# Optimization experiments

Measured on AMD Instinct MI355X. Metric: run time of the kernel, lower is better.

Reference implementation:

```python
import jax, jax.numpy as jnp
import numpy as np

E = 8      # num_expert
D = 1024   # d_model
H = 2048   # expert hidden (htoh4 size)
K = 2      # top_k
N = 2048   # tokens (batch*seq)


def setup_inputs() -> dict:
    key = jax.random.key(0)
    ks = jax.random.split(key, 4)
    sc = lambda k, shape, s: jax.random.normal(k, shape, jnp.float32) * s
    return {
        "inp": jax.random.normal(ks[0], (N, D), jnp.float32),
        "Wg": sc(ks[1], (D, E), D ** -0.5),          # NaiveGate linear
        "bg": jnp.zeros((E,), jnp.float32),
        "W1": sc(ks[2], (E, D, H), D ** -0.5),        # per-expert htoh4
        "b1": jnp.zeros((E, H), jnp.float32),
        "W2": sc(ks[3], (E, H, D), H ** -0.5),        # per-expert h4toh
        "b2": jnp.zeros((E, D), jnp.float32),
    }


def reference(inp, Wg, bg, W1, b1, W2, b2):
    # NaiveGate: linear -> top_k logits -> softmax over the k selected logits
    logits = inp @ Wg + bg                              # [N, E]
    top_val, top_idx = jax.lax.top_k(logits, K)         # [N, K]
    gate_score = jax.nn.softmax(top_val, axis=-1)       # [N, K]

    # Expert grouped compute. Reference computes every expert on every token
    # (exact math, no capacity dropping); combine selects the routed ones.
    h = jax.nn.gelu(jnp.einsum('nd,edh->neh', inp, W1) + b1)   # [N, E, H]
    y = jnp.einsum('neh,ehd->ned', h, W2) + b2                 # [N, E, D]

    # Combine: equivalent to bmm(gate_score[N,1,K], x[N,K,D]) after gather.
    comb = jnp.sum(jax.nn.one_hot(top_idx, E, dtype=inp.dtype)
                   * gate_score[..., None], axis=1)            # [N, E]
    return jnp.einsum('ne,ned->nd', comb, y)                   # [N, D]
```

## Files before the change

kernel.cpp:

```cpp
#include <hip/hip_runtime.h>
#include <math.h>

#define N_TOK 2048
#define DM    1024
#define HD    2048
#define NE    8
#define RMAX  5120
#define TMAX  40
#define KSPL  2

#define GATE_BLKS 512
#define XCVT_BLKS 1024
#define WCV2_BLKS 2048
#define PREP_BLKS (GATE_BLKS + XCVT_BLKS + WCV2_BLKS)

typedef short short8 __attribute__((ext_vector_type(8)));
typedef unsigned short u16x8 __attribute__((ext_vector_type(8)));
typedef float f32x4  __attribute__((ext_vector_type(4)));

__device__ inline unsigned short f2b(float f) {
  unsigned int u = __float_as_uint(f);
  return (unsigned short)((u + 0x7FFFu + ((u >> 16) & 1u)) >> 16);
}
__device__ inline float b2f(unsigned short s) {
  return __uint_as_float(((unsigned int)s) << 16);
}
__device__ inline void gload_lds16(const void* g, void* l) {
  __builtin_amdgcn_global_load_lds(
      (const __attribute__((address_space(1))) unsigned int*)g,
      (__attribute__((address_space(3))) unsigned int*)l, 16, 0, 0);
}

__global__ __launch_bounds__(256) void prep_kernel(
    const float* __restrict__ inp, const float* __restrict__ Wg,
    const float* __restrict__ bg,  const float* __restrict__ W2,
    int* __restrict__ top_idx, float* __restrict__ gate_w,
    unsigned short* __restrict__ Xb, unsigned short* __restrict__ W2C) {
  int bid = blockIdx.x;
  if (bid < GATE_BLKS) {
    int wave = threadIdx.x >> 6;
    int lane = threadIdx.x & 63;
    int n = bid * 4 + wave;
    float acc[NE];
#pragma unroll
    for (int e = 0; e < NE; ++e) acc[e] = 0.f;
    const float4* wg4 = reinterpret_cast<const float4*>(Wg);
#pragma unroll
    for (int i = 0; i < DM / 64; ++i) {
      int d = i * 64 + lane;
      float x = inp[n * DM + d];
      float4 w0 = wg4[d * 2 + 0];
      float4 w1 = wg4[d * 2 + 1];
      acc[0] += x * w0.x; acc[1] += x * w0.y; acc[2] += x * w0.z; acc[3] += x * w0.w;
      acc[4] += x * w1.x; acc[5] += x * w1.y; acc[6] += x * w1.z; acc[7] += x * w1.w;
    }
#pragma unroll
    for (int off = 32; off > 0; off >>= 1) {
#pragma unroll
      for (int e = 0; e < NE; ++e) acc[e] += __shfl_xor(acc[e], off);
    }
    if (lane == 0) {
      float v0 = -1e30f, v1 = -1e30f; int i0 = -1, i1 = -1;
#pragma unroll
      for (int e = 0; e < NE; ++e) {
        float v = acc[e] + bg[e];
        if (v > v0)      { v1 = v0; i1 = i0; v0 = v; i0 = e; }
        else if (v > v1) { v1 = v;  i1 = e; }
      }
      float e1 = expf(v1 - v0);
      float s  = 1.f + e1;
      top_idx[n * 2]     = i0;
      top_idx[n * 2 + 1] = i1;
      gate_w[n * 2]      = 1.f / s;
      gate_w[n * 2 + 1]  = e1 / s;
    }
  } else if (bid < GATE_BLKS + XCVT_BLKS) {
    int i = ((bid - GATE_BLKS) * 256 + threadIdx.x) * 8;
    float4 a = *(const float4*)(inp + i);
    float4 b = *(const float4*)(inp + i + 4);
    ushort4 pa, pb;
    pa.x = f2b(a.x); pa.y = f2b(a.y); pa.z = f2b(a.z); pa.w = f2b(a.w);
    pb.x = f2b(b.x); pb.y = f2b(b.y); pb.z = f2b(b.z); pb.w = f2b(b.w);
    *(ushort4*)(Xb + i)     = pa;
    *(ushort4*)(Xb + i + 4) = pb;
  } else {
    int wb = bid - (GATE_BLKS + XCVT_BLKS);
    int z  = wb >> 8;
    int r  = wb & 255;
    int gx = r & 3, gy = r >> 2;
    const float* src = W2 + (size_t)z * HD * DM;
    unsigned short* dst = W2C + (size_t)z * HD * DM;
    int n0 = gx * 256, k0 = gy * 32;
    int t  = threadIdx.x;
    int cg = t & 63, kg = t >> 6;
    const float* s = src + (size_t)(k0 + kg * 8) * DM + n0 + cg * 4;
    float4 v[8];
#pragma unroll
    for (int i = 0; i < 8; ++i) v[i] = *(const float4*)(s + (size_t)i * DM);
#pragma unroll
    for (int c = 0; c < 4; ++c) {
      u16x8 o;
      o[0] = f2b(v[0][c]); o[1] = f2b(v[1][c]); o[2] = f2b(v[2][c]); o[3] = f2b(v[3][c]);
      o[4] = f2b(v[4][c]); o[5] = f2b(v[5][c]); o[6] = f2b(v[6][c]); o[7] = f2b(v[7][c]);
      *(u16x8*)(dst + ((size_t)(k0 / 8 + kg) * DM + n0 + cg * 4 + c) * 8) = o;
    }
  }
}

__global__ __launch_bounds__(1024) void group_kernel(
    const int* __restrict__ top_idx,
    int* __restrict__ token_of, int* __restrict__ inv_g,
    int* __restrict__ tile_expert, int* __restrict__ tile_row0,
    int* __restrict__ n_tiles) {
  __shared__ int s_wtot[16];
  int tid = threadIdx.x, lane = tid & 63, wid = tid >> 6;
  int base = 0, tiles = 0;
  for (int e = 0; e < NE; ++e) {
    int cnt = 0;
#pragma unroll
    for (int c0 = 0; c0 < N_TOK; c0 += 1024) {
      int n = c0 + tid;
      int t0 = top_idx[n * 2], t1 = top_idx[n * 2 + 1];
      bool f = (t0 == e) || (t1 == e);
      int k = (t0 == e) ? 0 : 1;
      unsigned long long m = __ballot(f);
      int lp = __popcll(m & ((1ull << lane) - 1ull));
      if (lane == 0) s_wtot[wid] = __popcll(m);
      __syncthreads();
      int wbase = 0, tot = 0;
#pragma unroll
      for (int w = 0; w < 16; ++w) {
        int c = s_wtot[w];
        if (w < wid) wbase += c;
        tot += c;
      }
      if (f) {
        int pos = base + cnt + wbase + lp;
        token_of[pos] = n;
        inv_g[n * 2 + k] = pos;
      }
      cnt += tot;
      __syncthreads();
    }
    int padded = (cnt + 127) & ~127;
    for (int i = cnt + tid; i < padded; i += 1024) token_of[base + i] = -1;
    if (tid == 0) {
      for (int t = 0; t < padded / 128; ++t) {
        tile_expert[tiles + t] = e;
        tile_row0[tiles + t]   = base + t * 128;
      }
    }
    tiles += padded / 128;
    base  += padded;
    __syncthreads();
  }
  if (tid == 0) n_tiles[0] = tiles;
}

__global__ __launch_bounds__(256, 6) void ffn1_mfma(
    const unsigned short* __restrict__ Xb,
    const float* __restrict__ W1,
    const float* __restrict__ b1,
    const unsigned short* __restrict__ Xzero,
    const int* __restrict__ token_of, const int* __restrict__ tile_expert,
    const int* __restrict__ tile_row0, const int* __restrict__ n_tiles,
    unsigned short* __restrict__ Hbuf) {
  int lin  = blockIdx.x;
  int xcd  = lin & 7, slot = lin >> 3;
  int unit = xcd * 4 + slot / TMAX;
  int t    = slot % TMAX;
  if (t >= n_tiles[0]) return;
  int e    = tile_expert[t];
  int row0 = tile_row0[t];
  int h0   = unit * 64;
  __shared__ __align__(16) unsigned short Asl[2][128][32];
  __shared__ __align__(16) unsigned short Bsl[2][4][64][8];
  int tid = threadIdx.x, lane = tid & 63;
  int wid = tid >> 6, wr = wid >> 1, wc = wid & 1;
  int l15 = lane & 15, l4 = lane >> 4;
  int sw  = (l15 >> 1) & 3;

  int ar[2], asg[2], tk[2];
#pragma unroll
  for (int q = 0; q < 2; ++q) {
    int idx = tid + q * 256;
    ar[q]  = idx >> 2;
    asg[q] = (idx & 3) ^ ((ar[q] >> 1) & 3);
    tk[q]  = token_of[row0 + ar[q]];
  }
  int bcol = tid & 63, bks = tid >> 6;
  const float* W1e = W1 + (size_t)e * DM * HD;

  f32x4 acc[4][2] = {};
  float bvA[8], bvB[8];

  auto issueB = [&](int tt, float* bv) {
    const float* p = W1e + (size_t)(tt * 32 + bks * 8) * HD + h0 + bcol;
#pragma unroll
    for (int i = 0; i < 8; ++i) bv[i] = p[(size_t)i * HD];
  };
  auto packwrite = [&](const float* bv, int buf) {
    u16x8 o;
#pragma unroll
    for (int i = 0; i < 8; ++i) o[i] = f2b(bv[i]);
    *(u16x8*)&Bsl[buf][bks][bcol][0] = o;
  };
  auto issueA = [&](int tt, int buf) {
#pragma unroll
    for (int q = 0; q < 2; ++q) {
      int idx = tid + q * 256;
      const unsigned short* ga = (tk[q] < 0)
          ? Xzero
          : Xb + (size_t)tk[q] * DM + tt * 32 + asg[q] * 8;
      gload_lds16(ga, (char*)&Asl[buf][0][0] + (size_t)idx * 16);
    }
  };
  auto compute = [&](int buf) {
    short8 a[4], b[2];
#pragma unroll
    for (int m = 0; m < 4; ++m) {
      int R = wr * 64 + m * 16 + l15;
      a[m] = *(const short8*)((const char*)&Asl[buf][0][0] + R * 64 + ((l4 ^ sw) << 4));
    }
#pragma unroll
    for (int n = 0; n < 2; ++n)
      b[n] = *(const short8*)&Bsl[buf][l4][wc * 32 + n * 16 + l15][0];
#pragma unroll
    for (int m = 0; m < 4; ++m)
#pragma unroll
      for (int n = 0; n < 2; ++n)
        acc[m][n] = __builtin_amdgcn_mfma_f32_16x16x32_bf16(a[m], b[n], acc[m][n], 0, 0, 0);
  };

  issueB(0, bvA);
  issueA(0, 0);
  for (int kt = 0; kt < 32; kt += 2) {
    packwrite(bvA, 0);
    __syncthreads();
    if (kt + 1 < 32) { issueB(kt + 1, bvB); issueA(kt + 1, 1); }
    compute(0);
    packwrite(bvB, 1);
    __syncthreads();
    if (kt + 2 < 32) { issueB(kt + 2, bvA); issueA(kt + 2, 0); }
    compute(1);
  }

  float bias[2];
#pragma unroll
  for (int n = 0; n < 2; ++n) bias[n] = b1[e * HD + h0 + wc * 32 + n * 16 + l15];
#pragma unroll
  for (int m = 0; m < 4; ++m) {
#pragma unroll
    for (int n = 0; n < 2; ++n) {
      int col = h0 + wc * 32 + n * 16 + l15;
#pragma unroll
      for (int j = 0; j < 4; ++j) {
        int row = row0 + wr * 64 + m * 16 + l4 * 4 + j;
        float x = acc[m][n][j] + bias[n];
        float g = 0.5f * x * (1.f + tanhf(0.7978845608f * (x + 0.044715f * x * x * x)));
        Hbuf[(size_t)row * HD + col] = f2b(g);
      }
    }
  }
}

__global__ __launch_bounds__(256, 6) void ffn2_mfma(
    const unsigned short* __restrict__ Hbuf,
    const unsigned short* __restrict__ W2C,
    const float* __restrict__ b2,
    const int* __restrict__ tile_expert, const int* __restrict__ tile_row0,
    const int* __restrict__ n_tiles,
    float* __restrict__ Ypart) {
  int lin  = blockIdx.x;
  int xcd  = lin & 7, slot = lin >> 3;
  int unit = xcd * 4 + slot / TMAX;
  int t    = slot % TMAX;
  if (t >= n_tiles[0]) return;
  int e    = tile_expert[t];
  int row0 = tile_row0[t];
  int d0   = (unit >> 1) * 64;
  int ks   = unit & 1;
  int kbase = ks * (HD / KSPL);
  int kb0   = kbase >> 3;
  __shared__ __align__(16) unsigned short Asl[2][128][32];
  __shared__ __align__(16) unsigned short Bsl[2][4][64][8];
  int tid = threadIdx.x, lane = tid & 63;
  int wid = tid >> 6, wr = wid >> 1, wc = wid & 1;
  int l15 = lane & 15, l4 = lane >> 4;
  int sw  = (l15 >> 1) & 3;

  int ar[2], asg[2];
#pragma unroll
  for (int q = 0; q < 2; ++q) {
    int idx = tid + q * 256;
    ar[q]  = idx >> 2;
    asg[q] = (idx & 3) ^ ((ar[q] >> 1) & 3);
  }
  int bcol = tid & 63, bks = tid >> 6;
  const unsigned short* W2e = W2C + (size_t)e * HD * DM;

  f32x4 acc[4][2] = {};

  auto issueAB = [&](int tt, int buf) {
#pragma unroll
    for (int q = 0; q < 2; ++q) {
      int idx = tid + q * 256;
      const unsigned short* ga =
          Hbuf + (size_t)(row0 + ar[q]) * HD + kbase + tt * 32 + asg[q] * 8;
      gload_lds16(ga, (char*)&Asl[buf][0][0] + (size_t)idx * 16);
    }
    const unsigned short* gb =
        W2e + ((size_t)(kb0 + tt * 4 + bks) * DM + d0 + bcol) * 8;
    gload_lds16(gb, (char*)&Bsl[buf][0][0] + (size_t)tid * 16);
  };
  auto compute = [&](int buf) {
    short8 a[4], b[2];
#pragma unroll
    for (int m = 0; m < 4; ++m) {
      int R = wr * 64 + m * 16 + l15;
      a[m] = *(const short8*)((const char*)&Asl[buf][0][0] + R * 64 + ((l4 ^ sw) << 4));
    }
#pragma unroll
    for (int n = 0; n < 2; ++n)
      b[n] = *(const short8*)&Bsl[buf][l4][wc * 32 + n * 16 + l15][0];
#pragma unroll
    for (int m = 0; m < 4; ++m)
#pragma unroll
      for (int n = 0; n < 2; ++n)
        acc[m][n] = __builtin_amdgcn_mfma_f32_16x16x32_bf16(a[m], b[n], acc[m][n], 0, 0, 0);
  };

  const int NT = HD / KSPL / 32;
  issueAB(0, 0);
  for (int kt = 0; kt < NT; kt += 2) {
    __syncthreads();
    if (kt + 1 < NT) issueAB(kt + 1, 1);
    compute(0);
    __syncthreads();
    if (kt + 2 < NT) issueAB(kt + 2, 0);
    compute(1);
  }

  float bias[2];
#pragma unroll
  for (int n = 0; n < 2; ++n)
    bias[n] = (ks == 0) ? b2[e * DM + d0 + wc * 32 + n * 16 + l15] : 0.f;
  float* Yp = Ypart + (size_t)ks * RMAX * DM;
#pragma unroll
  for (int m = 0; m < 4; ++m) {
#pragma unroll
    for (int n = 0; n < 2; ++n) {
      int col = d0 + wc * 32 + n * 16 + l15;
#pragma unroll
      for (int j = 0; j < 4; ++j) {
        int row = row0 + wr * 64 + m * 16 + l4 * 4 + j;
        Yp[(size_t)row * DM + col] = acc[m][n][j] + bias[n];
      }
    }
  }
}

__global__ void combine_kernel(const float* __restrict__ Ypart,
                               const int* __restrict__ inv_g,
                               const float* __restrict__ gate_w,
                               float* __restrict__ out) {
  int n = blockIdx.x;
  int r0 = inv_g[n * 2], r1 = inv_g[n * 2 + 1];
  float g0 = gate_w[n * 2], g1 = gate_w[n * 2 + 1];
  int i = threadIdx.x;
  const float4* y00 = (const float4*)(Ypart + (size_t)r0 * DM);
  const float4* y01 = (const float4*)(Ypart + (size_t)(RMAX + r0) * DM);
  const float4* y10 = (const float4*)(Ypart + (size_t)r1 * DM);
  const float4* y11 = (const float4*)(Ypart + (size_t)(RMAX + r1) * DM);
  float4 a0 = y00[i], a1 = y01[i], b0 = y10[i], b1 = y11[i];
  float4 rv;
  rv.x = g0 * (a0.x + a1.x) + g1 * (b0.x + b1.x);
  rv.y = g0 * (a0.y + a1.y) + g1 * (b0.y + b1.y);
  rv.z = g0 * (a0.z + a1.z) + g1 * (b0.z + b1.z);
  rv.w = g0 * (a0.w + a1.w) + g1 * (b0.w + b1.w);
  *(float4*)(out + (size_t)n * DM + i * 4) = rv;
}

extern "C" void kernel_launch(void* const* d_in, const int* in_sizes, int n_in,
                              void* d_out, int out_size, void* d_ws, size_t ws_size,
                              hipStream_t stream) {
  const float* inp = (const float*)d_in[0];
  const float* Wg  = (const float*)d_in[1];
  const float* bg  = (const float*)d_in[2];
  const float* W1  = (const float*)d_in[3];
  const float* b1  = (const float*)d_in[4];
  const float* W2  = (const float*)d_in[5];
  const float* b2  = (const float*)d_in[6];
  float* out = (float*)d_out;

  char* ws = (char*)d_ws;
  size_t off = 0;
  auto alloc = [&](size_t bytes) {
    size_t o = off;
    off = (off + bytes + 255) & ~(size_t)255;
    return o;
  };
  int*   top_idx     = (int*)  (ws + alloc(N_TOK * 2 * sizeof(int)));
  float* gate_w      = (float*)(ws + alloc(N_TOK * 2 * sizeof(float)));
  int*   token_of    = (int*)  (ws + alloc(RMAX * sizeof(int)));
  int*   inv_g       = (int*)  (ws + alloc(N_TOK * 2 * sizeof(int)));
  int*   tile_expert = (int*)  (ws + alloc(TMAX * sizeof(int)));
  int*   tile_row0   = (int*)  (ws + alloc(TMAX * sizeof(int)));
  int*   n_tiles     = (int*)  (ws + alloc(sizeof(int)));
  unsigned short* Xzero = (unsigned short*)(ws + alloc(DM * 2));
  unsigned short* Xb    = (unsigned short*)(ws + alloc((size_t)N_TOK * DM * 2));
  unsigned short* W2C   = (unsigned short*)(ws + alloc((size_t)NE * HD * DM * 2));
  unsigned short* Hbuf  = (unsigned short*)(ws + alloc((size_t)RMAX * HD * 2));
  float*          Ypart = (float*)(ws + alloc((size_t)KSPL * RMAX * DM * 4));
  (void)ws_size;

  hipMemsetAsync(Xzero, 0, DM * 2, stream);
  prep_kernel<<<PREP_BLKS, 256, 0, stream>>>(inp, Wg, bg, W2,
                                             top_idx, gate_w, Xb, W2C);
  group_kernel<<<1, 1024, 0, stream>>>(top_idx, token_of, inv_g,
                                       tile_expert, tile_row0, n_tiles);
  ffn1_mfma<<<8 * 4 * TMAX, 256, 0, stream>>>(
      Xb, W1, b1, Xzero, token_of, tile_expert, tile_row0, n_tiles, Hbuf);
  ffn2_mfma<<<8 * 4 * TMAX, 256, 0, stream>>>(
      Hbuf, W2C, b2, tile_expert, tile_row0, n_tiles, Ypart);
  combine_kernel<<<N_TOK, 256, 0, stream>>>(Ypart, inv_g, gate_w, out);
}
```

Baseline: 149.4 us.

## Pre-convert W1 to packed bf16 and move W2 conversion into ffn1 launch

W1 is now converted once in the prep kernel into a k-packed bf16 layout, so ffn1 loads its B tiles straight into LDS with global_load_lds instead of loading fp32 into registers, converting and storing to LDS. The W2 conversion moves from the prep kernel into extra blocks appended to the ffn1 grid, so it can overlap with ffn1 work. The cost is an extra bf16 W1 workspace buffer and a full W1 conversion pass (read 64MB fp32, write 32MB) on the critical path before grouping.

Result: slower. 157.2 us (+5.2%).

```diff
diff --git a/kernel.cpp b/kernel.cpp
--- a/kernel.cpp
+++ b/kernel.cpp
@@ -11,8 +11,10 @@
 
 #define GATE_BLKS 512
 #define XCVT_BLKS 1024
+#define WCV1_BLKS 2048
+#define PREP_BLKS (GATE_BLKS + XCVT_BLKS + WCV1_BLKS)
+#define FFN1_BLKS (8 * 4 * TMAX)
 #define WCV2_BLKS 2048
-#define PREP_BLKS (GATE_BLKS + XCVT_BLKS + WCV2_BLKS)
 
 typedef short short8 __attribute__((ext_vector_type(8)));
 typedef unsigned short u16x8 __attribute__((ext_vector_type(8)));
@@ -31,11 +33,28 @@
       (__attribute__((address_space(3))) unsigned int*)l, 16, 0, 0);
 }
 
+__device__ inline void wcvt_tile(const float* __restrict__ src,
+                                 unsigned short* __restrict__ dst,
+                                 int N, int n0, int k0, int tid) {
+  int cg = tid & 63, kg = tid >> 6;
+  const float* s = src + (size_t)(k0 + kg * 8) * N + n0 + cg * 4;
+  float4 v[8];
+#pragma unroll
+  for (int i = 0; i < 8; ++i) v[i] = *(const float4*)(s + (size_t)i * N);
+#pragma unroll
+  for (int c = 0; c < 4; ++c) {
+    u16x8 o;
+    o[0] = f2b(v[0][c]); o[1] = f2b(v[1][c]); o[2] = f2b(v[2][c]); o[3] = f2b(v[3][c]);
+    o[4] = f2b(v[4][c]); o[5] = f2b(v[5][c]); o[6] = f2b(v[6][c]); o[7] = f2b(v[7][c]);
+    *(u16x8*)(dst + ((size_t)(k0 / 8 + kg) * N + n0 + cg * 4 + c) * 8) = o;
+  }
+}
+
 __global__ __launch_bounds__(256) void prep_kernel(
     const float* __restrict__ inp, const float* __restrict__ Wg,
-    const float* __restrict__ bg,  const float* __restrict__ W2,
+    const float* __restrict__ bg,  const float* __restrict__ W1,
     int* __restrict__ top_idx, float* __restrict__ gate_w,
-    unsigned short* __restrict__ Xb, unsigned short* __restrict__ W2C) {
+    unsigned short* __restrict__ Xb, unsigned short* __restrict__ W1C) {
   int bid = blockIdx.x;
   if (bid < GATE_BLKS) {
     int wave = threadIdx.x >> 6;
@@ -87,23 +106,9 @@
     int wb = bid - (GATE_BLKS + XCVT_BLKS);
     int z  = wb >> 8;
     int r  = wb & 255;
-    int gx = r & 3, gy = r >> 2;
-    const float* src = W2 + (size_t)z * HD * DM;
-    unsigned short* dst = W2C + (size_t)z * HD * DM;
-    int n0 = gx * 256, k0 = gy * 32;
-    int t  = threadIdx.x;
-    int cg = t & 63, kg = t >> 6;
-    const float* s = src + (size_t)(k0 + kg * 8) * DM + n0 + cg * 4;
-    float4 v[8];
-#pragma unroll
-    for (int i = 0; i < 8; ++i) v[i] = *(const float4*)(s + (size_t)i * DM);
-#pragma unroll
-    for (int c = 0; c < 4; ++c) {
-      u16x8 o;
-      o[0] = f2b(v[0][c]); o[1] = f2b(v[1][c]); o[2] = f2b(v[2][c]); o[3] = f2b(v[3][c]);
-      o[4] = f2b(v[4][c]); o[5] = f2b(v[5][c]); o[6] = f2b(v[6][c]); o[7] = f2b(v[7][c]);
-      *(u16x8*)(dst + ((size_t)(k0 / 8 + kg) * DM + n0 + cg * 4 + c) * 8) = o;
-    }
+    int gx = r & 7, gy = r >> 3;
+    wcvt_tile(W1 + (size_t)z * DM * HD, W1C + (size_t)z * DM * HD,
+              HD, gx * 256, gy * 32, threadIdx.x);
   }
 }
 
@@ -159,14 +164,24 @@
 
 __global__ __launch_bounds__(256, 6) void ffn1_mfma(
     const unsigned short* __restrict__ Xb,
-    const float* __restrict__ W1,
+    const unsigned short* __restrict__ W1C,
     const float* __restrict__ b1,
     const unsigned short* __restrict__ Xzero,
     const int* __restrict__ token_of, const int* __restrict__ tile_expert,
     const int* __restrict__ tile_row0, const int* __restrict__ n_tiles,
-    unsigned short* __restrict__ Hbuf) {
-  int lin  = blockIdx.x;
-  int xcd  = lin & 7, slot = lin >> 3;
+    unsigned short* __restrict__ Hbuf,
+    const float* __restrict__ W2, unsigned short* __restrict__ W2C) {
+  int bid = blockIdx.x;
+  if (bid >= FFN1_BLKS) {
+    int wb = bid - FFN1_BLKS;
+    int z  = wb >> 8;
+    int r  = wb & 255;
+    int gx = r & 3, gy = r >> 2;
+    wcvt_tile(W2 + (size_t)z * HD * DM, W2C + (size_t)z * HD * DM,
+              DM, gx * 256, gy * 32, threadIdx.x);
+    return;
+  }
+  int xcd  = bid & 7, slot = bid >> 3;
   int unit = xcd * 4 + slot / TMAX;
   int t    = slot % TMAX;
   if (t >= n_tiles[0]) return;
@@ -189,23 +204,11 @@
     tk[q]  = token_of[row0 + ar[q]];
   }
   int bcol = tid & 63, bks = tid >> 6;
-  const float* W1e = W1 + (size_t)e * DM * HD;
+  const unsigned short* W1e = W1C + (size_t)e * DM * HD;
 
   f32x4 acc[4][2] = {};
-  float bvA[8], bvB[8];
-
-  auto issueB = [&](int tt, float* bv) {
-    const float* p = W1e + (size_t)(tt * 32 + bks * 8) * HD + h0 + bcol;
-#pragma unroll
-    for (int i = 0; i < 8; ++i) bv[i] = p[(size_t)i * HD];
-  };
-  auto packwrite = [&](const float* bv, int buf) {
-    u16x8 o;
-#pragma unroll
-    for (int i = 0; i < 8; ++i) o[i] = f2b(bv[i]);
-    *(u16x8*)&Bsl[buf][bks][bcol][0] = o;
-  };
-  auto issueA = [&](int tt, int buf) {
+
+  auto issueAB = [&](int tt, int buf) {
 #pragma unroll
     for (int q = 0; q < 2; ++q) {
       int idx = tid + q * 256;
@@ -214,6 +217,9 @@
           : Xb + (size_t)tk[q] * DM + tt * 32 + asg[q] * 8;
       gload_lds16(ga, (char*)&Asl[buf][0][0] + (size_t)idx * 16);
     }
+    const unsigned short* gb =
+        W1e + ((size_t)(tt * 4 + bks) * HD + h0 + bcol) * 8;
+    gload_lds16(gb, (char*)&Bsl[buf][0][0] + (size_t)tid * 16);
   };
   auto compute = [&](int buf) {
     short8 a[4], b[2];
@@ -232,16 +238,13 @@
         acc[m][n] = __builtin_amdgcn_mfma_f32_16x16x32_bf16(a[m], b[n], acc[m][n], 0, 0, 0);
   };
 
-  issueB(0, bvA);
-  issueA(0, 0);
+  issueAB(0, 0);
   for (int kt = 0; kt < 32; kt += 2) {
-    packwrite(bvA, 0);
     __syncthreads();
-    if (kt + 1 < 32) { issueB(kt + 1, bvB); issueA(kt + 1, 1); }
+    if (kt + 1 < 32) issueAB(kt + 1, 1);
     compute(0);
-    packwrite(bvB, 1);
     __syncthreads();
-    if (kt + 2 < 32) { issueB(kt + 2, bvA); issueA(kt + 2, 0); }
+    if (kt + 2 < 32) issueAB(kt + 2, 0);
     compute(1);
   }
 
@@ -409,18 +412,20 @@
   int*   n_tiles     = (int*)  (ws + alloc(sizeof(int)));
   unsigned short* Xzero = (unsigned short*)(ws + alloc(DM * 2));
   unsigned short* Xb    = (unsigned short*)(ws + alloc((size_t)N_TOK * DM * 2));
+  unsigned short* W1C   = (unsigned short*)(ws + alloc((size_t)NE * DM * HD * 2));
   unsigned short* W2C   = (unsigned short*)(ws + alloc((size_t)NE * HD * DM * 2));
   unsigned short* Hbuf  = (unsigned short*)(ws + alloc((size_t)RMAX * HD * 2));
   float*          Ypart = (float*)(ws + alloc((size_t)KSPL * RMAX * DM * 4));
   (void)ws_size;
 
   hipMemsetAsync(Xzero, 0, DM * 2, stream);
-  prep_kernel<<<PREP_BLKS, 256, 0, stream>>>(inp, Wg, bg, W2,
-                                             top_idx, gate_w, Xb, W2C);
+  prep_kernel<<<PREP_BLKS, 256, 0, stream>>>(inp, Wg, bg, W1,
+                                             top_idx, gate_w, Xb, W1C);
   group_kernel<<<1, 1024, 0, stream>>>(top_idx, token_of, inv_g,
                                        tile_expert, tile_row0, n_tiles);
-  ffn1_mfma<<<8 * 4 * TMAX, 256, 0, stream>>>(
-      Xb, W1, b1, Xzero, token_of, tile_expert, tile_row0, n_tiles, Hbuf);
+  ffn1_mfma<<<FFN1_BLKS + WCV2_BLKS, 256, 0, stream>>>(
+      Xb, W1C, b1, Xzero, token_of, tile_expert, tile_row0, n_tiles, Hbuf,
+      W2, W2C);
   ffn2_mfma<<<8 * 4 * TMAX, 256, 0, stream>>>(
       Hbuf, W2C, b2, tile_expert, tile_row0, n_tiles, Ypart);
   combine_kernel<<<N_TOK, 256, 0, stream>>>(Ypart, inv_g, gate_w, out);
```
